# Kernel optimization log

Measured on AMD Instinct MI355X. Metric: run time of the kernel, lower is better.

## Reference

```python
import jax, jax.numpy as jnp
import numpy as np

N = 1024
DIM = 3
H = 64  # hidden width from sizes=[64, 64]


def _mlp(inp, W1, b1, W2, b2, W3, b3):
    # hk.nets.MLP(sizes + [1], activation=softplus): activate all but last layer
    h = jax.nn.softplus(inp @ W1 + b1)
    h = jax.nn.softplus(h @ W2 + b2)
    return h @ W3 + b3


def setup_inputs() -> dict:
    key = jax.random.key(0)
    ks = jax.random.split(key, 14)
    x = jax.random.normal(ks[0], (N, DIM), dtype=jnp.float32)
    t = jax.random.uniform(ks[1], (), dtype=jnp.float32)
    s = 0.01  # TruncatedNormal(0.01) init
    return {
        "x": x,
        "t": t,
        "xi_W1": jax.random.normal(ks[2], (2, H), jnp.float32) * s,
        "xi_b1": jnp.zeros((H,), jnp.float32),
        "xi_W2": jax.random.normal(ks[3], (H, H), jnp.float32) * s,
        "xi_b2": jnp.zeros((H,), jnp.float32),
        "xi_W3": jax.random.normal(ks[4], (H, 1), jnp.float32) * s,
        "xi_b3": jnp.zeros((1,), jnp.float32),
        "eta_W1": jax.random.normal(ks[5], (2, H), jnp.float32) * s,
        "eta_b1": jnp.zeros((H,), jnp.float32),
        "eta_W2": jax.random.normal(ks[6], (H, H), jnp.float32) * s,
        "eta_b2": jnp.zeros((H,), jnp.float32),
        "eta_W3": jax.random.normal(ks[7], (H, 1), jnp.float32) * s,
        "eta_b3": jnp.zeros((1,), jnp.float32),
    }


def reference(x, t, xi_W1, xi_b1, xi_W2, xi_b2, xi_W3, xi_b3,
              eta_W1, eta_b1, eta_W2, eta_b2, eta_W3, eta_b3):
    n = x.shape[0]
    # one-body term: xi(|x_i|, t) * x_i
    r = jnp.linalg.norm(x, axis=-1)  # (n,)
    inp_xi = jnp.stack([r, jnp.full_like(r, t)], axis=-1)  # (n, 2)
    res = _mlp(inp_xi, xi_W1, xi_b1, xi_W2, xi_b2, xi_W3, xi_b3) * x  # (n, dim)
    # two-body term: sum_j eta(|x_i - x_j|, t) * (x_i - x_j)
    rij = x[:, None, :] - x[None, :, :]  # (n, n, dim)
    eye = jnp.eye(n, dtype=x.dtype)
    rdist = jnp.linalg.norm(rij + eye[..., None], axis=-1) * (1.0 - eye)  # (n, n)
    inp_eta = jnp.stack([rdist, jnp.full_like(rdist, t)], axis=-1)  # (n, n, 2)
    eta_out = _mlp(inp_eta, eta_W1, eta_b1, eta_W2, eta_b2, eta_W3, eta_b3)  # (n, n, 1)
    res = res + (eta_out * rij).sum(axis=1)
    return res
```

## Files before the change

### kernel.cpp

```cpp
#include <hip/hip_runtime.h>
#include <math.h>


#define TABLE_N 512
#define RMAX 16.0f
#define NPART 1024
#define EBLK 65
#define XBLK 128
#define DELTA (RMAX / (float)TABLE_N)
#define FLAG_OFF 1024
#define FLAG_MAGIC 0x9E3779B9u

__device__ __forceinline__ float sp_fast(float v) {
    return __logf(1.f + __expf(v));
}

__global__ __launch_bounds__(256, 1) void k_fused(
    const float* __restrict__ x, const float* __restrict__ t_ptr,
    const float* __restrict__ xiW1, const float* __restrict__ xib1,
    const float* __restrict__ xiW2, const float* __restrict__ xib2,
    const float* __restrict__ xiW3, const float* __restrict__ xib3,
    const float* __restrict__ eW1,  const float* __restrict__ eb1,
    const float* __restrict__ eW2,  const float* __restrict__ eb2,
    const float* __restrict__ eW3,  const float* __restrict__ eb3,
    float* __restrict__ ws, float* __restrict__ out)
{
    __shared__ __align__(16) float w2s[4096];
    __shared__ __align__(16) float w1s[128];
    __shared__ __align__(16) float b1s[64];
    __shared__ __align__(16) float b2s[64];
    __shared__ __align__(16) float w3s[64];
    __shared__ __align__(16) float hbuf[4][128];
    __shared__ __align__(16) float xsoa[3 * NPART];
    __shared__ __align__(16) float tab[516];

    const int tid = threadIdx.x;
    const int b   = blockIdx.x;
    const bool tb = (b < EBLK);

    const float* __restrict__ W1 = tb ? eW1 : xiW1;
    const float* __restrict__ B1 = tb ? eb1 : xib1;
    const float* __restrict__ W2 = tb ? eW2 : xiW2;
    const float* __restrict__ B2 = tb ? eb2 : xib2;
    const float* __restrict__ W3 = tb ? eW3 : xiW3;

    {
        const float4* src = (const float4*)W2;
        float4* dst = (float4*)w2s;
        #pragma unroll
        for (int i2 = 0; i2 < 4; ++i2) dst[tid + 256 * i2] = src[tid + 256 * i2];
        if (tid < 128)      w1s[tid]       = W1[tid];
        else if (tid < 192) b1s[tid - 128] = B1[tid - 128];
        else                b2s[tid - 192] = B2[tid - 192];
        if (tid < 64)       w3s[tid]       = W3[tid];
    }
    if (!tb) {
        const float4* src = (const float4*)x;
        float4* dst = (float4*)xsoa;
        #pragma unroll
        for (int i2 = 0; i2 < 3; ++i2) dst[tid + 256 * i2] = src[tid + 256 * i2];
    }

    const float t  = t_ptr[0];
    const float B3 = tb ? eb3[0] : xib3[0];
    const int lane = tid & 63;
    const int w    = tid >> 6;
    const int e0   = (tb ? 8 * b : 8 * (b - EBLK)) + 2 * w;
    const int e1   = e0 + 1;

    float r0, r1;
    if (tb) {
        r0 = (float)e0 * DELTA;
        r1 = (float)e1 * DELTA;
    } else {
        float ax_ = x[3 * e0], ay_ = x[3 * e0 + 1], az_ = x[3 * e0 + 2];
        float bx_ = x[3 * e1], by_ = x[3 * e1 + 1], bz_ = x[3 * e1 + 2];
        r0 = sqrtf(fmaf(ax_, ax_, fmaf(ay_, ay_, az_ * az_)));
        r1 = sqrtf(fmaf(bx_, bx_, fmaf(by_, by_, bz_ * bz_)));
    }
    __syncthreads();

    const float w1a = w1s[lane], w1b = w1s[64 + lane], b1v = b1s[lane];
    hbuf[w][lane]      = sp_fast(fmaf(r0, w1a, fmaf(t, w1b, b1v)));
    hbuf[w][64 + lane] = sp_fast(fmaf(r1, w1a, fmaf(t, w1b, b1v)));
    float z0 = b2s[lane], z1 = z0;
    #pragma unroll
    for (int k = 0; k < 64; k += 4) {
        float4 ha = *(const float4*)&hbuf[w][k];
        float4 hb = *(const float4*)&hbuf[w][64 + k];
        float wa  = w2s[k * 64 + lane];
        float wbv = w2s[(k + 1) * 64 + lane];
        float wc  = w2s[(k + 2) * 64 + lane];
        float wd  = w2s[(k + 3) * 64 + lane];
        z0 = fmaf(ha.x, wa,  z0); z1 = fmaf(hb.x, wa,  z1);
        z0 = fmaf(ha.y, wbv, z0); z1 = fmaf(hb.y, wbv, z1);
        z0 = fmaf(ha.z, wc,  z0); z1 = fmaf(hb.z, wc,  z1);
        z0 = fmaf(ha.w, wd,  z0); z1 = fmaf(hb.w, wd,  z1);
    }
    float q0 = sp_fast(z0) * w3s[lane];
    float q1 = sp_fast(z1) * w3s[lane];
    #pragma unroll
    for (int off = 32; off > 0; off >>= 1) {
        q0 += __shfl_xor(q0, off);
        q1 += __shfl_xor(q1, off);
    }
    const float f0 = q0 + B3;
    const float f1 = q1 + B3;

    if (tb) {
        if (lane == 0) {
            if (e0 <= TABLE_N)
                __hip_atomic_store(&ws[e0], f0, __ATOMIC_RELAXED,
                                   __HIP_MEMORY_SCOPE_AGENT);
            if (e1 <= TABLE_N)
                __hip_atomic_store(&ws[e1], f1, __ATOMIC_RELAXED,
                                   __HIP_MEMORY_SCOPE_AGENT);
        }
        __syncthreads();
        if (tid == 0) {
            __hip_atomic_store((unsigned int*)ws + FLAG_OFF + b, FLAG_MAGIC,
                               __ATOMIC_RELAXED, __HIP_MEMORY_SCOPE_AGENT);
        }
        return;
    }

    if (tid < EBLK) {
        const unsigned int* fl = (const unsigned int*)ws + FLAG_OFF + tid;
        unsigned int v = __hip_atomic_load(fl, __ATOMIC_RELAXED,
                                           __HIP_MEMORY_SCOPE_AGENT);
        int it = 0;
        while (v != FLAG_MAGIC) {
            __builtin_amdgcn_s_sleep(1);
            v = ((++it & 31) == 0)
                  ? __hip_atomic_load(fl, __ATOMIC_ACQUIRE,
                                      __HIP_MEMORY_SCOPE_AGENT)
                  : __hip_atomic_load(fl, __ATOMIC_RELAXED,
                                      __HIP_MEMORY_SCOPE_AGENT);
        }
    }
    __syncthreads();
    {
        float v0 = __hip_atomic_load(&ws[tid], __ATOMIC_RELAXED,
                                     __HIP_MEMORY_SCOPE_AGENT);
        float v1 = __hip_atomic_load(&ws[tid + 256], __ATOMIC_RELAXED,
                                     __HIP_MEMORY_SCOPE_AGENT);
        tab[tid]       = v0;
        tab[tid + 256] = v1;
        if (tid == 0)
            tab[512] = __hip_atomic_load(&ws[512], __ATOMIC_RELAXED,
                                         __HIP_MEMORY_SCOPE_AGENT);
    }
    __syncthreads();

    const float xi0 = xsoa[3 * e0], yi0 = xsoa[3 * e0 + 1], zi0 = xsoa[3 * e0 + 2];
    const float xi1 = xsoa[3 * e1], yi1 = xsoa[3 * e1 + 1], zi1 = xsoa[3 * e1 + 2];
    float ax0 = 0.f, ay0 = 0.f, az0 = 0.f;
    float ax1 = 0.f, ay1 = 0.f, az1 = 0.f;
    const float scale = (float)TABLE_N / RMAX;
    #pragma unroll
    for (int it = 0; it < NPART / 64; ++it) {
        int j = it * 64 + lane;
        float xj = xsoa[3 * j], yj = xsoa[3 * j + 1], zj = xsoa[3 * j + 2];
        {
            float dx = xi0 - xj, dy = yi0 - yj, dz = zi0 - zj;
            float r = sqrtf(fmaf(dx, dx, fmaf(dy, dy, dz * dz)));
            float u = fminf(r * scale, (float)TABLE_N - 0.001f);
            int i0 = (int)u;
            float fr = u - (float)i0;
            float t0 = tab[i0], t1v = tab[i0 + 1];
            float f = fmaf(fr, t1v - t0, t0);
            ax0 = fmaf(f, dx, ax0); ay0 = fmaf(f, dy, ay0); az0 = fmaf(f, dz, az0);
        }
        {
            float dx = xi1 - xj, dy = yi1 - yj, dz = zi1 - zj;
            float r = sqrtf(fmaf(dx, dx, fmaf(dy, dy, dz * dz)));
            float u = fminf(r * scale, (float)TABLE_N - 0.001f);
            int i0 = (int)u;
            float fr = u - (float)i0;
            float t0 = tab[i0], t1v = tab[i0 + 1];
            float f = fmaf(fr, t1v - t0, t0);
            ax1 = fmaf(f, dx, ax1); ay1 = fmaf(f, dy, ay1); az1 = fmaf(f, dz, az1);
        }
    }
    #pragma unroll
    for (int off = 32; off > 0; off >>= 1) {
        ax0 += __shfl_xor(ax0, off); ay0 += __shfl_xor(ay0, off); az0 += __shfl_xor(az0, off);
        ax1 += __shfl_xor(ax1, off); ay1 += __shfl_xor(ay1, off); az1 += __shfl_xor(az1, off);
    }
    if (lane == 0) {
        out[3 * e0]     = fmaf(f0, xi0, ax0);
        out[3 * e0 + 1] = fmaf(f0, yi0, ay0);
        out[3 * e0 + 2] = fmaf(f0, zi0, az0);
        out[3 * e1]     = fmaf(f1, xi1, ax1);
        out[3 * e1 + 1] = fmaf(f1, yi1, ay1);
        out[3 * e1 + 2] = fmaf(f1, zi1, az1);
    }
}

extern "C" void kernel_launch(void* const* d_in, const int* in_sizes, int n_in,
                              void* d_out, int out_size, void* d_ws, size_t ws_size,
                              hipStream_t stream) {
    const float* x     = (const float*)d_in[0];
    const float* t     = (const float*)d_in[1];
    const float* xiW1  = (const float*)d_in[2];
    const float* xib1  = (const float*)d_in[3];
    const float* xiW2  = (const float*)d_in[4];
    const float* xib2  = (const float*)d_in[5];
    const float* xiW3  = (const float*)d_in[6];
    const float* xib3  = (const float*)d_in[7];
    const float* eW1   = (const float*)d_in[8];
    const float* eb1   = (const float*)d_in[9];
    const float* eW2   = (const float*)d_in[10];
    const float* eb2   = (const float*)d_in[11];
    const float* eW3   = (const float*)d_in[12];
    const float* eb3   = (const float*)d_in[13];
    float* out = (float*)d_out;
    float* ws  = (float*)d_ws;

    k_fused<<<EBLK + XBLK, 256, 0, stream>>>(
        x, t, xiW1, xib1, xiW2, xib2, xiW3, xib3,
        eW1, eb1, eW2, eb2, eW3, eb3, ws, out);
}
```

Measured before the change: 86.81 us.

## Use 512-thread blocks, one particle per wave, per-wave table-ready flags

Blocks grow to 512 threads. Table producer blocks drop from 65 to 33, and each wave now writes its own ready flag, so consumers poll 264 flags instead of waiting on a block-level barrier. Consumer blocks assign one particle per wave instead of two, so 128 blocks of 8 waves cover the 1024 particles with half the per-wave pair work and more waves to hide latency. The risk is more flag polling traffic and a lower register budget per thread at 512 threads.

```diff
diff --git a/kernel.cpp b/kernel.cpp
--- a/kernel.cpp
+++ b/kernel.cpp
@@ -5,8 +5,9 @@
 #define TABLE_N 512
 #define RMAX 16.0f
 #define NPART 1024
-#define EBLK 65
+#define PBLK 33
 #define XBLK 128
+#define NFLAGS 264
 #define DELTA (RMAX / (float)TABLE_N)
 #define FLAG_OFF 1024
 #define FLAG_MAGIC 0x9E3779B9u
@@ -15,7 +16,7 @@
     return __logf(1.f + __expf(v));
 }
 
-__global__ __launch_bounds__(256, 1) void k_fused(
+__global__ __launch_bounds__(512, 1) void k_fused(
     const float* __restrict__ x, const float* __restrict__ t_ptr,
     const float* __restrict__ xiW1, const float* __restrict__ xib1,
     const float* __restrict__ xiW2, const float* __restrict__ xib2,
@@ -30,13 +31,13 @@
     __shared__ __align__(16) float b1s[64];
     __shared__ __align__(16) float b2s[64];
     __shared__ __align__(16) float w3s[64];
-    __shared__ __align__(16) float hbuf[4][128];
+    __shared__ __align__(16) float hbuf[8][128];
     __shared__ __align__(16) float xsoa[3 * NPART];
     __shared__ __align__(16) float tab[516];
 
     const int tid = threadIdx.x;
     const int b   = blockIdx.x;
-    const bool tb = (b < EBLK);
+    const bool tb = (b < PBLK);
 
     const float* __restrict__ W1 = tb ? eW1 : xiW1;
     const float* __restrict__ B1 = tb ? eb1 : xib1;
@@ -47,84 +48,91 @@
     {
         const float4* src = (const float4*)W2;
         float4* dst = (float4*)w2s;
-        #pragma unroll
-        for (int i2 = 0; i2 < 4; ++i2) dst[tid + 256 * i2] = src[tid + 256 * i2];
+        dst[tid]       = src[tid];
+        dst[tid + 512] = src[tid + 512];
         if (tid < 128)      w1s[tid]       = W1[tid];
         else if (tid < 192) b1s[tid - 128] = B1[tid - 128];
-        else                b2s[tid - 192] = B2[tid - 192];
-        if (tid < 64)       w3s[tid]       = W3[tid];
+        else if (tid < 256) b2s[tid - 192] = B2[tid - 192];
+        else if (tid < 320) w3s[tid - 256] = W3[tid - 256];
     }
     if (!tb) {
         const float4* src = (const float4*)x;
         float4* dst = (float4*)xsoa;
-        #pragma unroll
-        for (int i2 = 0; i2 < 3; ++i2) dst[tid + 256 * i2] = src[tid + 256 * i2];
+        dst[tid] = src[tid];
+        if (tid < 256) dst[tid + 512] = src[tid + 512];
     }
 
     const float t  = t_ptr[0];
     const float B3 = tb ? eb3[0] : xib3[0];
     const int lane = tid & 63;
     const int w    = tid >> 6;
-    const int e0   = (tb ? 8 * b : 8 * (b - EBLK)) + 2 * w;
-    const int e1   = e0 + 1;
-
-    float r0, r1;
+    __syncthreads();
+
     if (tb) {
-        r0 = (float)e0 * DELTA;
-        r1 = (float)e1 * DELTA;
-    } else {
-        float ax_ = x[3 * e0], ay_ = x[3 * e0 + 1], az_ = x[3 * e0 + 2];
-        float bx_ = x[3 * e1], by_ = x[3 * e1 + 1], bz_ = x[3 * e1 + 2];
-        r0 = sqrtf(fmaf(ax_, ax_, fmaf(ay_, ay_, az_ * az_)));
-        r1 = sqrtf(fmaf(bx_, bx_, fmaf(by_, by_, bz_ * bz_)));
-    }
-    __syncthreads();
+        const int e0 = 16 * b + 2 * w;
+        const int e1 = e0 + 1;
+        const float r0 = (float)e0 * DELTA;
+        const float r1 = (float)e1 * DELTA;
+        const float w1a = w1s[lane], w1b = w1s[64 + lane], b1v = b1s[lane];
+        hbuf[w][lane]      = sp_fast(fmaf(r0, w1a, fmaf(t, w1b, b1v)));
+        hbuf[w][64 + lane] = sp_fast(fmaf(r1, w1a, fmaf(t, w1b, b1v)));
+        float z0 = b2s[lane], z1 = z0;
+        #pragma unroll
+        for (int k = 0; k < 64; k += 4) {
+            float4 ha = *(const float4*)&hbuf[w][k];
+            float4 hb = *(const float4*)&hbuf[w][64 + k];
+            float wa  = w2s[k * 64 + lane];
+            float wbv = w2s[(k + 1) * 64 + lane];
+            float wc  = w2s[(k + 2) * 64 + lane];
+            float wd  = w2s[(k + 3) * 64 + lane];
+            z0 = fmaf(ha.x, wa,  z0); z1 = fmaf(hb.x, wa,  z1);
+            z0 = fmaf(ha.y, wbv, z0); z1 = fmaf(hb.y, wbv, z1);
+            z0 = fmaf(ha.z, wc,  z0); z1 = fmaf(hb.z, wc,  z1);
+            z0 = fmaf(ha.w, wd,  z0); z1 = fmaf(hb.w, wd,  z1);
+        }
+        float q0 = sp_fast(z0) * w3s[lane];
+        float q1 = sp_fast(z1) * w3s[lane];
+        #pragma unroll
+        for (int off = 32; off > 0; off >>= 1) {
+            q0 += __shfl_xor(q0, off);
+            q1 += __shfl_xor(q1, off);
+        }
+        if (lane == 0) {
+            if (e0 <= TABLE_N)
+                __hip_atomic_store(&ws[e0], q0 + B3, __ATOMIC_RELAXED,
+                                   __HIP_MEMORY_SCOPE_AGENT);
+            if (e1 <= TABLE_N)
+                __hip_atomic_store(&ws[e1], q1 + B3, __ATOMIC_RELAXED,
+                                   __HIP_MEMORY_SCOPE_AGENT);
+            asm volatile("s_waitcnt vmcnt(0)" ::: "memory");
+            __hip_atomic_store((unsigned int*)ws + FLAG_OFF + 8 * b + w,
+                               FLAG_MAGIC, __ATOMIC_RELAXED,
+                               __HIP_MEMORY_SCOPE_AGENT);
+        }
+        return;
+    }
+
+    const int i = 8 * (b - PBLK) + w;
+    const float xi0 = xsoa[3 * i], yi0 = xsoa[3 * i + 1], zi0 = xsoa[3 * i + 2];
+    const float r0 = sqrtf(fmaf(xi0, xi0, fmaf(yi0, yi0, zi0 * zi0)));
 
     const float w1a = w1s[lane], w1b = w1s[64 + lane], b1v = b1s[lane];
-    hbuf[w][lane]      = sp_fast(fmaf(r0, w1a, fmaf(t, w1b, b1v)));
-    hbuf[w][64 + lane] = sp_fast(fmaf(r1, w1a, fmaf(t, w1b, b1v)));
-    float z0 = b2s[lane], z1 = z0;
+    hbuf[w][lane] = sp_fast(fmaf(r0, w1a, fmaf(t, w1b, b1v)));
+    float z0 = b2s[lane];
     #pragma unroll
     for (int k = 0; k < 64; k += 4) {
         float4 ha = *(const float4*)&hbuf[w][k];
-        float4 hb = *(const float4*)&hbuf[w][64 + k];
-        float wa  = w2s[k * 64 + lane];
-        float wbv = w2s[(k + 1) * 64 + lane];
-        float wc  = w2s[(k + 2) * 64 + lane];
-        float wd  = w2s[(k + 3) * 64 + lane];
-        z0 = fmaf(ha.x, wa,  z0); z1 = fmaf(hb.x, wa,  z1);
-        z0 = fmaf(ha.y, wbv, z0); z1 = fmaf(hb.y, wbv, z1);
-        z0 = fmaf(ha.z, wc,  z0); z1 = fmaf(hb.z, wc,  z1);
-        z0 = fmaf(ha.w, wd,  z0); z1 = fmaf(hb.w, wd,  z1);
+        z0 = fmaf(ha.x, w2s[k * 64 + lane],       z0);
+        z0 = fmaf(ha.y, w2s[(k + 1) * 64 + lane], z0);
+        z0 = fmaf(ha.z, w2s[(k + 2) * 64 + lane], z0);
+        z0 = fmaf(ha.w, w2s[(k + 3) * 64 + lane], z0);
     }
     float q0 = sp_fast(z0) * w3s[lane];
-    float q1 = sp_fast(z1) * w3s[lane];
-    #pragma unroll
-    for (int off = 32; off > 0; off >>= 1) {
-        q0 += __shfl_xor(q0, off);
-        q1 += __shfl_xor(q1, off);
-    }
-    const float f0 = q0 + B3;
-    const float f1 = q1 + B3;
-
-    if (tb) {
-        if (lane == 0) {
-            if (e0 <= TABLE_N)
-                __hip_atomic_store(&ws[e0], f0, __ATOMIC_RELAXED,
-                                   __HIP_MEMORY_SCOPE_AGENT);
-            if (e1 <= TABLE_N)
-                __hip_atomic_store(&ws[e1], f1, __ATOMIC_RELAXED,
-                                   __HIP_MEMORY_SCOPE_AGENT);
-        }
-        __syncthreads();
-        if (tid == 0) {
-            __hip_atomic_store((unsigned int*)ws + FLAG_OFF + b, FLAG_MAGIC,
-                               __ATOMIC_RELAXED, __HIP_MEMORY_SCOPE_AGENT);
-        }
-        return;
-    }
-
-    if (tid < EBLK) {
+    #pragma unroll
+    for (int off = 32; off > 0; off >>= 1) q0 += __shfl_xor(q0, off);
+    const float fxi = q0 + B3;
+
+    if (tid < NFLAGS) {
         const unsigned int* fl = (const unsigned int*)ws + FLAG_OFF + tid;
         unsigned int v = __hip_atomic_load(fl, __ATOMIC_RELAXED,
                                            __HIP_MEMORY_SCOPE_AGENT);
@@ -140,60 +148,42 @@
     }
     __syncthreads();
     {
-        float v0 = __hip_atomic_load(&ws[tid], __ATOMIC_RELAXED,
+        tab[tid] = __hip_atomic_load(&ws[tid], __ATOMIC_RELAXED,
                                      __HIP_MEMORY_SCOPE_AGENT);
-        float v1 = __hip_atomic_load(&ws[tid + 256], __ATOMIC_RELAXED,
-                                     __HIP_MEMORY_SCOPE_AGENT);
-        tab[tid]       = v0;
-        tab[tid + 256] = v1;
         if (tid == 0)
             tab[512] = __hip_atomic_load(&ws[512], __ATOMIC_RELAXED,
                                          __HIP_MEMORY_SCOPE_AGENT);
     }
     __syncthreads();
 
-    const float xi0 = xsoa[3 * e0], yi0 = xsoa[3 * e0 + 1], zi0 = xsoa[3 * e0 + 2];
-    const float xi1 = xsoa[3 * e1], yi1 = xsoa[3 * e1 + 1], zi1 = xsoa[3 * e1 + 2];
-    float ax0 = 0.f, ay0 = 0.f, az0 = 0.f;
-    float ax1 = 0.f, ay1 = 0.f, az1 = 0.f;
+    float ax = 0.f, ay = 0.f, az = 0.f;
     const float scale = (float)TABLE_N / RMAX;
     #pragma unroll
     for (int it = 0; it < NPART / 64; ++it) {
         int j = it * 64 + lane;
-        float xj = xsoa[3 * j], yj = xsoa[3 * j + 1], zj = xsoa[3 * j + 2];
-        {
-            float dx = xi0 - xj, dy = yi0 - yj, dz = zi0 - zj;
-            float r = sqrtf(fmaf(dx, dx, fmaf(dy, dy, dz * dz)));
-            float u = fminf(r * scale, (float)TABLE_N - 0.001f);
-            int i0 = (int)u;
-            float fr = u - (float)i0;
-            float t0 = tab[i0], t1v = tab[i0 + 1];
-            float f = fmaf(fr, t1v - t0, t0);
-            ax0 = fmaf(f, dx, ax0); ay0 = fmaf(f, dy, ay0); az0 = fmaf(f, dz, az0);
-        }
-        {
-            float dx = xi1 - xj, dy = yi1 - yj, dz = zi1 - zj;
-            float r = sqrtf(fmaf(dx, dx, fmaf(dy, dy, dz * dz)));
-            float u = fminf(r * scale, (float)TABLE_N - 0.001f);
-            int i0 = (int)u;
-            float fr = u - (float)i0;
-            float t0 = tab[i0], t1v = tab[i0 + 1];
-            float f = fmaf(fr, t1v - t0, t0);
-            ax1 = fmaf(f, dx, ax1); ay1 = fmaf(f, dy, ay1); az1 = fmaf(f, dz, az1);
-        }
+        float dx = xi0 - xsoa[3 * j];
+        float dy = yi0 - xsoa[3 * j + 1];
+        float dz = zi0 - xsoa[3 * j + 2];
+        float r = sqrtf(fmaf(dx, dx, fmaf(dy, dy, dz * dz)));
+        float u = fminf(r * scale, (float)TABLE_N - 0.001f);
+        int i0 = (int)u;
+        float fr = u - (float)i0;
+        float t0 = tab[i0], t1v = tab[i0 + 1];
+        float f = fmaf(fr, t1v - t0, t0);
+        ax = fmaf(f, dx, ax);
+        ay = fmaf(f, dy, ay);
+        az = fmaf(f, dz, az);
     }
     #pragma unroll
     for (int off = 32; off > 0; off >>= 1) {
-        ax0 += __shfl_xor(ax0, off); ay0 += __shfl_xor(ay0, off); az0 += __shfl_xor(az0, off);
-        ax1 += __shfl_xor(ax1, off); ay1 += __shfl_xor(ay1, off); az1 += __shfl_xor(az1, off);
+        ax += __shfl_xor(ax, off);
+        ay += __shfl_xor(ay, off);
+        az += __shfl_xor(az, off);
     }
     if (lane == 0) {
-        out[3 * e0]     = fmaf(f0, xi0, ax0);
-        out[3 * e0 + 1] = fmaf(f0, yi0, ay0);
-        out[3 * e0 + 2] = fmaf(f0, zi0, az0);
-        out[3 * e1]     = fmaf(f1, xi1, ax1);
-        out[3 * e1 + 1] = fmaf(f1, yi1, ay1);
-        out[3 * e1 + 2] = fmaf(f1, zi1, az1);
+        out[3 * i]     = fmaf(fxi, xi0, ax);
+        out[3 * i + 1] = fmaf(fxi, yi0, ay);
+        out[3 * i + 2] = fmaf(fxi, zi0, az);
     }
 }
 
@@ -217,7 +207,7 @@
     float* out = (float*)d_out;
     float* ws  = (float*)d_ws;
 
-    k_fused<<<EBLK + XBLK, 256, 0, stream>>>(
+    k_fused<<<PBLK + XBLK, 512, 0, stream>>>(
         x, t, xiW1, xib1, xiW2, xib2, xiW3, xib3,
         eW1, eb1, eW2, eb2, eW3, eb3, ws, out);
 }
```

After: 85.15 us. No clear change (-1.9%).
